# Kernel optimization log

Hardware: AMD Instinct MI355X
Metric: run time of the kernel (lower is better)

Reference implementation:

```python
import jax, jax.numpy as jnp
import numpy as np

N = 100000      # num nodes
E = 1600000     # num edges
DIN, DH, DOUT = 128, 64, 32
BN_EPS = 1e-5


def setup_inputs() -> dict:
    key = jax.random.key(0)
    ks = jax.random.split(key, 6)

    def xavier(k, fi, fo):
        lim = np.sqrt(6.0 / (fi + fo)).astype(np.float32)
        return jax.random.uniform(k, (fi, fo), jnp.float32, -lim, lim)

    return {
        "x": jax.random.normal(ks[0], (N, DIN), jnp.float32),
        "edge_index": jax.random.randint(ks[1], (2, E), 0, N, dtype=jnp.int32),
        "W1": xavier(ks[2], DIN, DH),
        "b1": jnp.zeros((DH,), jnp.float32),
        "gamma1": jnp.ones((DH,), jnp.float32),
        "beta1": jnp.zeros((DH,), jnp.float32),
        "W2": xavier(ks[3], DH, DOUT),
        "b2": jnp.zeros((DOUT,), jnp.float32),
    }


def _gcn_norm(edge_index, n, dtype):
    # add self-loops, then symmetric normalization deg^-1/2[src] * deg^-1/2[dst]
    loop = jnp.arange(n, dtype=edge_index.dtype)
    src = jnp.concatenate([edge_index[0], loop])
    dst = jnp.concatenate([edge_index[1], loop])
    deg = jax.ops.segment_sum(jnp.ones_like(dst, dtype=dtype), dst, num_segments=n)
    dis = 1.0 / jnp.sqrt(deg)  # deg >= 1 due to self-loops
    norm = dis[src] * dis[dst]
    return src, dst, norm


def _gcn_layer(h, W, b, src, dst, norm, n):
    h = h @ W
    msg = h[src] * norm[:, None]                       # [E+N, d] gather
    out = jax.ops.segment_sum(msg, dst, num_segments=n)  # scatter-add
    return out + b


def reference(x, edge_index, W1, b1, gamma1, beta1, W2, b2):
    src, dst, norm = _gcn_norm(edge_index, N, x.dtype)
    # layer 1: GCNConv -> BatchNorm (batch stats) -> ReLU (dropout = eval/identity)
    h = _gcn_layer(x, W1, b1, src, dst, norm, N)
    mean = h.mean(axis=0)
    var = h.var(axis=0)
    h = (h - mean) / jnp.sqrt(var + BN_EPS) * gamma1 + beta1
    h = jax.nn.relu(h)
    # layer 2: GCNConv -> node embeddings [N, DOUT]
    out = _gcn_layer(h, W2, b2, src, dst, norm, N)
    return out
```

## Files before the change

kernel.cpp:

```cpp
#include <hip/hip_runtime.h>

#define DIN 128
#define DH 64
#define DOUT 32
#define BN_EPS 1e-5f

#define BK 128
#define BKSH 7
#define NBK_MAX 784
#define G 256
#define CAP 2560
#define CCAP 3584

typedef __attribute__((ext_vector_type(8))) short short8;
typedef __attribute__((ext_vector_type(4))) float floatx4;

__device__ __forceinline__ unsigned short f2bf(float f) {
    union { float f; unsigned u; } v; v.f = f;
    unsigned r = (v.u + 0x7FFFu + ((v.u >> 16) & 1u)) >> 16;
    return (unsigned short)r;
}
__device__ __forceinline__ float bf2f(unsigned short h) {
    union { unsigned u; float f; } v; v.u = ((unsigned)h) << 16;
    return v.f;
}
__device__ __forceinline__ float lo_f(unsigned u) {
    union { unsigned u; float f; } v; v.u = u << 16;
    return v.f;
}
__device__ __forceinline__ float hi_f(unsigned u) {
    union { unsigned u; float f; } v; v.u = u & 0xFFFF0000u;
    return v.f;
}
__device__ __forceinline__ unsigned pack2bf(float lo, float hi) {
    return (unsigned)f2bf(lo) | ((unsigned)f2bf(hi) << 16);
}


__global__ __launch_bounds__(512) void hist_k(const int* __restrict__ dst, int* __restrict__ hist_g,
                                              int E, int nbk, int chunk) {
    __shared__ int hist[NBK_MAX];
    int g = blockIdx.x, tid = threadIdx.x;
    for (int b = tid; b < nbk; b += 512) hist[b] = 0;
    __syncthreads();
    int i0 = g * chunk, iend = min(i0 + chunk, E);
    for (int i = i0 + tid; i < iend; i += 512)
        atomicAdd(&hist[dst[i] >> BKSH], 1);
    __syncthreads();
    for (int b = tid; b < nbk; b += 512)
        hist_g[(size_t)g * nbk + b] = hist[b];
}


__global__ __launch_bounds__(256) void scan_k(const int* __restrict__ hist_g, int* __restrict__ rowoff,
                                              int* __restrict__ tot, int nbk) {
    __shared__ int seg[16][17];
    int tid = threadIdx.x;
    int gl = tid >> 4, bl = tid & 15;
    int b = blockIdx.x * 16 + bl;
    bool bok = b < nbk;
    int vals[16];
    int psum = 0;
    #pragma unroll
    for (int j = 0; j < 16; j++) {
        int g = gl * 16 + j;
        int v = bok ? hist_g[(size_t)g * nbk + b] : 0;
        vals[j] = v; psum += v;
    }
    seg[gl][bl] = psum;
    __syncthreads();
    #pragma unroll
    for (int off = 1; off < 16; off <<= 1) {
        int t = (gl >= off) ? seg[gl - off][bl] : 0;
        __syncthreads();
        seg[gl][bl] += t;
        __syncthreads();
    }
    int run = seg[gl][bl] - psum;
    if (gl == 15 && bok) tot[b] = seg[15][bl];
    #pragma unroll
    for (int j = 0; j < 16; j++) {
        int g = gl * 16 + j;
        if (bok) rowoff[(size_t)g * nbk + b] = run;
        run += vals[j];
    }
}


__global__ __launch_bounds__(512) void scatter_k(const int* __restrict__ src, const int* __restrict__ dst,
                                                 const int* __restrict__ rowoff,
                                                 unsigned* __restrict__ recs, int E, int nbk, int chunk) {
    __shared__ int cur[NBK_MAX];
    int g = blockIdx.x, tid = threadIdx.x;
    for (int b = tid; b < nbk; b += 512)
        cur[b] = b * CAP + rowoff[(size_t)g * nbk + b];
    __syncthreads();
    int i0 = g * chunk, iend = min(i0 + chunk, E);
    for (int i = i0 + tid; i < iend; i += 512) {
        int s = src[i], d = dst[i];
        int b = d >> BKSH;
        int slot = atomicAdd(&cur[b], 1);
        if (slot < (b + 1) * CAP)
            recs[slot] = ((unsigned)s << BKSH) | (unsigned)(d & (BK - 1));
    }
}


__global__ __launch_bounds__(512) void csr_k(const unsigned* __restrict__ recs, const int* __restrict__ tot,
                                             float* __restrict__ dis, int2* __restrict__ rpde,
                                             int* __restrict__ col, int n) {
    __shared__ int deg8[8][BK];
    __shared__ int wb[8][BK];
    __shared__ int deg[BK], sc[BK], bas[BK];
    int b = blockIdx.x, tid = threadIdx.x;
    int w = tid >> 6, lane = tid & 63;
    for (int i = tid; i < 8 * BK; i += 512) ((int*)deg8)[i] = 0;
    __syncthreads();
    int lo = b * CAP;
    int clo = b * CCAP;
    int ne = min(tot[b], CAP);
    int hi = lo + ne;
    for (int e = lo + w * 64 + lane; e < hi; e += 512)
        atomicAdd(&deg8[w][recs[e] & (BK - 1)], 1);
    __syncthreads();
    if (tid < BK) {
        int run = 0;
        #pragma unroll
        for (int ww = 0; ww < 8; ww++) { wb[ww][tid] = run; run += deg8[ww][tid]; }
        deg[tid] = run;
        sc[tid] = (run + 7) & ~7;
    }
    __syncthreads();
    for (int off = 1; off < BK; off <<= 1) {
        int t = (tid < BK && tid >= off) ? sc[tid - off] : 0;
        __syncthreads();
        if (tid < BK) sc[tid] += t;
        __syncthreads();
    }
    if (tid < BK) {
        int d = deg[tid];
        int pdeg = (d + 7) & ~7;
        int base = sc[tid] - pdeg;
        bas[tid] = base;
        int g = b * BK + tid;
        if (g < n) {
            dis[g] = rsqrtf((float)(d + 1));
            rpde[g] = make_int2(clo + base, d);
        }
        for (int j = d; j < pdeg; j++)
            col[clo + base + j] = n;
    }
    __syncthreads();
    for (int i = tid; i < 8 * BK; i += 512)
        ((int*)wb)[i] += bas[i & (BK - 1)];
    __syncthreads();
    for (int e = lo + w * 64 + lane; e < hi; e += 512) {
        unsigned r = recs[e];
        int dl = r & (BK - 1);
        int k = atomicAdd(&wb[w][dl], 1);
        col[clo + k] = (int)(r >> BKSH);
    }
}


__global__ __launch_bounds__(256) void gemm1_k(const float* __restrict__ x,
                                               const float* __restrict__ W1,
                                               const float* __restrict__ dis,
                                               unsigned short* __restrict__ h1s, int n, int np1) {
    __shared__ unsigned short xb[64][136];
    __shared__ unsigned short wt[64][136];
    int tid = threadIdx.x;
    int r0b = blockIdx.x * 64;

    for (int c = tid; c < 2048; c += 256) {
        int k = c >> 4, n4 = (c & 15) * 4;
        float4 v = ((const float4*)W1)[c];
        wt[n4 + 0][k] = f2bf(v.x);
        wt[n4 + 1][k] = f2bf(v.y);
        wt[n4 + 2][k] = f2bf(v.z);
        wt[n4 + 3][k] = f2bf(v.w);
    }
    for (int c = tid; c < 2048; c += 256) {
        int r = c >> 5, k4 = (c & 31) * 4;
        int gr = r0b + r;
        float4 v = make_float4(0.f, 0.f, 0.f, 0.f);
        if (gr < n) v = ((const float4*)x)[(gr << 5) + (k4 >> 2)];
        ushort4 o;
        o.x = f2bf(v.x); o.y = f2bf(v.y); o.z = f2bf(v.z); o.w = f2bf(v.w);
        *(ushort4*)&xb[r][k4] = o;
    }
    __syncthreads();

    int w = tid >> 6, lane = tid & 63;
    int rr = lane & 15, q = lane >> 4;
    floatx4 acc0 = {0.f, 0.f, 0.f, 0.f}, acc1 = acc0, acc2 = acc0, acc3 = acc0;
    #pragma unroll
    for (int kt = 0; kt < 4; kt++) {
        int k0 = kt * 32 + q * 8;
        short8 a  = *(const short8*)&xb[w * 16 + rr][k0];
        short8 b0 = *(const short8*)&wt[rr][k0];
        short8 b1 = *(const short8*)&wt[16 + rr][k0];
        short8 b2 = *(const short8*)&wt[32 + rr][k0];
        short8 b3 = *(const short8*)&wt[48 + rr][k0];
        acc0 = __builtin_amdgcn_mfma_f32_16x16x32_bf16(a, b0, acc0, 0, 0, 0);
        acc1 = __builtin_amdgcn_mfma_f32_16x16x32_bf16(a, b1, acc1, 0, 0, 0);
        acc2 = __builtin_amdgcn_mfma_f32_16x16x32_bf16(a, b2, acc2, 0, 0, 0);
        acc3 = __builtin_amdgcn_mfma_f32_16x16x32_bf16(a, b3, acc3, 0, 0, 0);
    }
    #pragma unroll
    for (int t = 0; t < 4; t++) {
        int gr = r0b + w * 16 + q * 4 + t;
        if (gr < n) {
            float dd = dis[gr];
            h1s[(size_t)0 * np1 * 16 + gr * 16 + rr] = f2bf(acc0[t] * dd);
            h1s[(size_t)1 * np1 * 16 + gr * 16 + rr] = f2bf(acc1[t] * dd);
            h1s[(size_t)2 * np1 * 16 + gr * 16 + rr] = f2bf(acc2[t] * dd);
            h1s[(size_t)3 * np1 * 16 + gr * 16 + rr] = f2bf(acc3[t] * dd);
        } else if (gr == n) {
            h1s[(size_t)0 * np1 * 16 + gr * 16 + rr] = 0;
            h1s[(size_t)1 * np1 * 16 + gr * 16 + rr] = 0;
            h1s[(size_t)2 * np1 * 16 + gr * 16 + rr] = 0;
            h1s[(size_t)3 * np1 * 16 + gr * 16 + rr] = 0;
        }
    }
}


__global__ __launch_bounds__(256) void agg1_k(const unsigned* __restrict__ h1p,
                                              const int2* __restrict__ rpde,
                                              const int* __restrict__ col,
                                              unsigned* __restrict__ outp, int n, int np1, int nh) {
    int b = blockIdx.x;
    int slot = b & 7;
    int q = slot >> 1, hn = slot & 1;
    int wv = threadIdx.x >> 6;
    int lane = threadIdx.x & 63;
    int half = lane >> 5, hl = lane & 31;
    int f = hl & 3, eslot = hl >> 2;
    int node = hn * nh + (b >> 3) * 8 + wv * 2 + half;
    if (node >= n) return;

    int2 rd = rpde[node];
    int e = rd.x, dg = rd.y;
    int pm = ((dg + 7) & ~7) - 1;

    const uint2* qt = (const uint2*)h1p + (size_t)q * np1 * 4;

    int i0 = eslot, i1 = 8 + eslot, i2 = 16 + eslot, i3 = 24 + eslot;
    int s0 = col[e + min(i0, pm)];
    int s1 = col[e + min(i1, pm)];
    int s2 = col[e + min(i2, pm)];
    int s3 = col[e + min(i3, pm)];
    s0 = (i0 <= pm) ? s0 : n;
    s1 = (i1 <= pm) ? s1 : n;
    s2 = (i2 <= pm) ? s2 : n;
    s3 = (i3 <= pm) ? s3 : n;
    uint2 u0 = qt[s0 * 4 + f];
    uint2 u1 = qt[s1 * 4 + f];
    uint2 u2 = qt[s2 * 4 + f];
    uint2 u3 = qt[s3 * 4 + f];
    uint2 us = qt[node * 4 + f];
    __builtin_amdgcn_sched_barrier(0);

    float xl = (lo_f(u0.x) + lo_f(u1.x)) + (lo_f(u2.x) + lo_f(u3.x));
    float xh = (hi_f(u0.x) + hi_f(u1.x)) + (hi_f(u2.x) + hi_f(u3.x));
    float yl = (lo_f(u0.y) + lo_f(u1.y)) + (lo_f(u2.y) + lo_f(u3.y));
    float yh = (hi_f(u0.y) + hi_f(u1.y)) + (hi_f(u2.y) + hi_f(u3.y));

    if (pm >= 32) {
        for (int bb = 32; bb <= pm; bb += 8) {
            int s = col[e + bb + eslot];
            uint2 u = qt[s * 4 + f];
            xl += lo_f(u.x); xh += hi_f(u.x);
            yl += lo_f(u.y); yh += hi_f(u.y);
        }
    }

    xl += __shfl_xor(xl, 4, 64); xl += __shfl_xor(xl, 8, 64); xl += __shfl_xor(xl, 16, 64);
    xh += __shfl_xor(xh, 4, 64); xh += __shfl_xor(xh, 8, 64); xh += __shfl_xor(xh, 16, 64);
    yl += __shfl_xor(yl, 4, 64); yl += __shfl_xor(yl, 8, 64); yl += __shfl_xor(yl, 16, 64);
    yh += __shfl_xor(yh, 4, 64); yh += __shfl_xor(yh, 8, 64); yh += __shfl_xor(yh, 16, 64);

    if (eslot == 0) {
        float dn = rsqrtf((float)(dg + 1));
        uint2 o;
        o.x = pack2bf((xl + lo_f(us.x)) * dn, (xh + hi_f(us.x)) * dn);
        o.y = pack2bf((yl + lo_f(us.y)) * dn, (yh + hi_f(us.y)) * dn);
        ((uint2*)outp)[((size_t)q * n + node) * 4 + f] = o;
    }
}


__global__ __launch_bounds__(256) void bnstats_k(const unsigned short* __restrict__ agg1b,
                                                 float* __restrict__ stats, int n) {
    int fidx = threadIdx.x & 63, g = threadIdx.x >> 6;
    int qq = fidx >> 4, fi = fidx & 15;
    const unsigned short* base = agg1b + (size_t)qq * n * 16 + fi;
    float sum = 0.f, sq = 0.f;
    for (int r = blockIdx.x * 4 + g; r < n; r += gridDim.x * 4) {
        float v = bf2f(base[(size_t)r * 16]);
        sum += v; sq += v * v;
    }
    __shared__ float s1[4][64], s2[4][64];
    s1[g][fidx] = sum; s2[g][fidx] = sq;
    __syncthreads();
    if (g == 0) {
        sum = s1[0][fidx] + s1[1][fidx] + s1[2][fidx] + s1[3][fidx];
        sq  = s2[0][fidx] + s2[1][fidx] + s2[2][fidx] + s2[3][fidx];
        atomicAdd(&stats[fidx], sum);
        atomicAdd(&stats[64 + fidx], sq);
    }
}


__global__ __launch_bounds__(256) void gemm2_k(const unsigned short* __restrict__ agg1b,
                                               const float* __restrict__ W2,
                                               const float* __restrict__ stats,
                                               const float* __restrict__ gamma, const float* __restrict__ beta,
                                               const float* __restrict__ dis,
                                               unsigned short* __restrict__ h2s, float invn, int n, int np1) {
    __shared__ unsigned short ab[64][72];
    __shared__ unsigned short wt[32][72];
    __shared__ float s_s[64], s_t[64];
    int tid = threadIdx.x;
    int r0b = blockIdx.x * 64;
    if (tid < 64) {
        float mean = stats[tid] * invn;
        float var = stats[64 + tid] * invn - mean * mean;
        float s = gamma[tid] * rsqrtf(var + BN_EPS);
        s_s[tid] = s;
        s_t[tid] = beta[tid] - mean * s;
    }
    for (int c = tid; c < 512; c += 256) {
        int k = c >> 3, n4 = (c & 7) * 4;
        float4 v = ((const float4*)W2)[c];
        wt[n4 + 0][k] = f2bf(v.x);
        wt[n4 + 1][k] = f2bf(v.y);
        wt[n4 + 2][k] = f2bf(v.z);
        wt[n4 + 3][k] = f2bf(v.w);
    }
    __syncthreads();
    for (int c = tid; c < 512; c += 256) {
        int r = c >> 3, k0 = (c & 7) * 8;
        int gr = r0b + r;
        unsigned short tmp[8];
        if (gr < n) {
            const unsigned short* ap = &agg1b[(size_t)(k0 >> 4) * n * 16 + gr * 16 + (k0 & 8)];
            #pragma unroll
            for (int j = 0; j < 8; j++)
                tmp[j] = f2bf(fmaxf(bf2f(ap[j]) * s_s[k0 + j] + s_t[k0 + j], 0.f));
        } else {
            #pragma unroll
            for (int j = 0; j < 8; j++) tmp[j] = 0;
        }
        *(short8*)&ab[r][k0] = *(short8*)tmp;
    }
    __syncthreads();

    int w = tid >> 6, lane = tid & 63;
    int rr = lane & 15, q = lane >> 4;
    floatx4 acc0 = {0.f, 0.f, 0.f, 0.f}, acc1 = acc0;
    #pragma unroll
    for (int kt = 0; kt < 2; kt++) {
        int k0 = kt * 32 + q * 8;
        short8 a  = *(const short8*)&ab[w * 16 + rr][k0];
        short8 b0 = *(const short8*)&wt[rr][k0];
        short8 b1 = *(const short8*)&wt[16 + rr][k0];
        acc0 = __builtin_amdgcn_mfma_f32_16x16x32_bf16(a, b0, acc0, 0, 0, 0);
        acc1 = __builtin_amdgcn_mfma_f32_16x16x32_bf16(a, b1, acc1, 0, 0, 0);
    }
    #pragma unroll
    for (int t = 0; t < 4; t++) {
        int gr = r0b + w * 16 + q * 4 + t;
        if (gr < n) {
            float dd = dis[gr];
            h2s[(size_t)0 * np1 * 16 + gr * 16 + rr] = f2bf(acc0[t] * dd);
            h2s[(size_t)1 * np1 * 16 + gr * 16 + rr] = f2bf(acc1[t] * dd);
        } else if (gr == n) {
            h2s[(size_t)0 * np1 * 16 + gr * 16 + rr] = 0;
            h2s[(size_t)1 * np1 * 16 + gr * 16 + rr] = 0;
        }
    }
}


__global__ __launch_bounds__(256) void agg2_k(const unsigned* __restrict__ h2p,
                                              const int2* __restrict__ rpde,
                                              const int* __restrict__ col, const float* __restrict__ b2,
                                              float* __restrict__ out, int n, int np1, int nq) {
    int b = blockIdx.x;
    int slot = b & 7;
    int h = slot >> 2, qn = slot & 3;
    int wv = threadIdx.x >> 6;
    int lane = threadIdx.x & 63;
    int half = lane >> 5, hl = lane & 31;
    int f = hl & 3, eslot = hl >> 2;
    int node = qn * nq + (b >> 3) * 8 + wv * 2 + half;
    if (node >= n) return;

    int2 rd = rpde[node];
    int e = rd.x, dg = rd.y;
    int pm = ((dg + 7) & ~7) - 1;

    const uint2* ht = (const uint2*)h2p + (size_t)h * np1 * 4;

    int i0 = eslot, i1 = 8 + eslot, i2 = 16 + eslot, i3 = 24 + eslot;
    int s0 = col[e + min(i0, pm)];
    int s1 = col[e + min(i1, pm)];
    int s2 = col[e + min(i2, pm)];
    int s3 = col[e + min(i3, pm)];
    s0 = (i0 <= pm) ? s0 : n;
    s1 = (i1 <= pm) ? s1 : n;
    s2 = (i2 <= pm) ? s2 : n;
    s3 = (i3 <= pm) ? s3 : n;
    uint2 u0 = ht[s0 * 4 + f];
    uint2 u1 = ht[s1 * 4 + f];
    uint2 u2 = ht[s2 * 4 + f];
    uint2 u3 = ht[s3 * 4 + f];
    uint2 us = ht[node * 4 + f];
    __builtin_amdgcn_sched_barrier(0);

    float xl = (lo_f(u0.x) + lo_f(u1.x)) + (lo_f(u2.x) + lo_f(u3.x));
    float xh = (hi_f(u0.x) + hi_f(u1.x)) + (hi_f(u2.x) + hi_f(u3.x));
    float yl = (lo_f(u0.y) + lo_f(u1.y)) + (lo_f(u2.y) + lo_f(u3.y));
    float yh = (hi_f(u0.y) + hi_f(u1.y)) + (hi_f(u2.y) + hi_f(u3.y));

    if (pm >= 32) {
        for (int bb = 32; bb <= pm; bb += 8) {
            int s = col[e + bb + eslot];
            uint2 u = ht[s * 4 + f];
            xl += lo_f(u.x); xh += hi_f(u.x);
            yl += lo_f(u.y); yh += hi_f(u.y);
        }
    }

    xl += __shfl_xor(xl, 4, 64); xl += __shfl_xor(xl, 8, 64); xl += __shfl_xor(xl, 16, 64);
    xh += __shfl_xor(xh, 4, 64); xh += __shfl_xor(xh, 8, 64); xh += __shfl_xor(xh, 16, 64);
    yl += __shfl_xor(yl, 4, 64); yl += __shfl_xor(yl, 8, 64); yl += __shfl_xor(yl, 16, 64);
    yh += __shfl_xor(yh, 4, 64); yh += __shfl_xor(yh, 8, 64); yh += __shfl_xor(yh, 16, 64);

    if (eslot == 0) {
        float dn = rsqrtf((float)(dg + 1));
        float4 bb4 = ((const float4*)b2)[h * 4 + f];
        float4 o;
        o.x = (xl + lo_f(us.x)) * dn + bb4.x;
        o.y = (xh + hi_f(us.x)) * dn + bb4.y;
        o.z = (yl + lo_f(us.y)) * dn + bb4.z;
        o.w = (yh + hi_f(us.y)) * dn + bb4.w;
        ((float4*)out)[(size_t)node * 8 + h * 4 + f] = o;
    }
}


extern "C" void kernel_launch(void* const* d_in, const int* in_sizes, int n_in,
                              void* d_out, int out_size, void* d_ws, size_t ws_size,
                              hipStream_t stream) {
    const float* x      = (const float*)d_in[0];
    const int*   ei     = (const int*)d_in[1];
    const float* W1     = (const float*)d_in[2];
    const float* gamma1 = (const float*)d_in[4];
    const float* beta1  = (const float*)d_in[5];
    const float* W2     = (const float*)d_in[6];
    const float* b2     = (const float*)d_in[7];
    float* out = (float*)d_out;

    int N = in_sizes[0] / DIN;
    int E = in_sizes[1] / 2;
    const int* src = ei;
    const int* dst = ei + E;
    int nbk = (N + BK - 1) >> BKSH;
    int chunk = (E + G - 1) / G;
    int np1 = N + 1;

    size_t off = 0;
    auto alloc = [&](size_t elems) -> void* {
        void* p = (char*)d_ws + off * 4;
        off += (elems + 127) & ~size_t(127);
        return p;
    };
    int*            hist_g = (int*)alloc((size_t)G * NBK_MAX);
    int*            rowoff = (int*)alloc((size_t)G * NBK_MAX);
    int*            tot    = (int*)alloc(NBK_MAX);
    unsigned*       recs   = (unsigned*)alloc((size_t)NBK_MAX * CAP);
    int*            col    = (int*)alloc((size_t)NBK_MAX * CCAP);
    float*          dis    = (float*)alloc(N);
    int2*           rpde   = (int2*)alloc((size_t)N * 2);
    float*          stats  = (float*)alloc(128);
    unsigned short* h1s    = (unsigned short*)alloc((size_t)np1 * DH / 2);
    unsigned short* agg1b  = (unsigned short*)alloc((size_t)N * DH / 2);
    unsigned short* h2s    = h1s;

    hipMemsetAsync(stats, 0, 128 * sizeof(float), stream);

    hist_k<<<G, 512, 0, stream>>>(dst, hist_g, E, nbk, chunk);
    scan_k<<<(nbk + 15) / 16, 256, 0, stream>>>(hist_g, rowoff, tot, nbk);
    scatter_k<<<G, 512, 0, stream>>>(src, dst, rowoff, recs, E, nbk, chunk);
    csr_k<<<nbk, 512, 0, stream>>>(recs, tot, dis, rpde, col, N);

    gemm1_k<<<(N + 63) / 64, 256, 0, stream>>>(x, W1, dis, h1s, N, np1);

    int nh = (N + 1) / 2;
    int agg1_blocks = 8 * ((nh + 7) / 8);
    agg1_k<<<agg1_blocks, 256, 0, stream>>>((const unsigned*)h1s, rpde, col, (unsigned*)agg1b,
                                            N, np1, nh);

    bnstats_k<<<400, 256, 0, stream>>>(agg1b, stats, N);

    gemm2_k<<<(N + 63) / 64, 256, 0, stream>>>(agg1b, W2, stats, gamma1, beta1, dis, h2s,
                                               1.0f / (float)N, N, np1);

    int nqn = (N + 3) / 4;
    int agg2_blocks = 8 * ((nqn + 7) / 8);
    agg2_k<<<agg2_blocks, 256, 0, stream>>>((const unsigned*)h2s, rpde, col, b2, out,
                                            N, np1, nqn);
}
```

Baseline: 288.7 us.

## Assign one node per 4-lane group in aggregation kernels, dropping cross-lane reductions

The aggregation kernels now map 16 nodes per wavefront, with 4 lanes per node each owning a feature chunk. Each lane walks all of its node's edges serially in unrolled groups of 8, up to the wave-wide maximum degree, so the shuffle reductions go away. CSR padding becomes (d+8)&~7 so every row has at least one pad entry, which lets overrun indices clamp onto it. This trades intra-node edge parallelism for more nodes per wave and fewer reductions, but a single high-degree node now stalls its whole wave (degree divergence), and per-lane load latency chains get longer.

Measured after the change: 271.6 us. 5.9% less time.

```diff
diff --git a/kernel.cpp b/kernel.cpp
--- a/kernel.cpp
+++ b/kernel.cpp
@@ -128,7 +128,7 @@
         #pragma unroll
         for (int ww = 0; ww < 8; ww++) { wb[ww][tid] = run; run += deg8[ww][tid]; }
         deg[tid] = run;
-        sc[tid] = (run + 7) & ~7;
+        sc[tid] = (run + 8) & ~7;
     }
     __syncthreads();
     for (int off = 1; off < BK; off <<= 1) {
@@ -139,7 +139,7 @@
     }
     if (tid < BK) {
         int d = deg[tid];
-        int pdeg = (d + 7) & ~7;
+        int pdeg = (d + 8) & ~7;
         int base = sc[tid] - pdeg;
         bas[tid] = base;
         int g = b * BK + tid;
@@ -235,57 +235,41 @@
     int q = slot >> 1, hn = slot & 1;
     int wv = threadIdx.x >> 6;
     int lane = threadIdx.x & 63;
-    int half = lane >> 5, hl = lane & 31;
-    int f = hl & 3, eslot = hl >> 2;
-    int node = hn * nh + (b >> 3) * 8 + wv * 2 + half;
-    if (node >= n) return;
-
-    int2 rd = rpde[node];
-    int e = rd.x, dg = rd.y;
-    int pm = ((dg + 7) & ~7) - 1;
+    int ns = lane >> 2, f = lane & 3;
+    int node = hn * nh + (b >> 3) * 64 + wv * 16 + ns;
+    bool ok = node < n;
+    int nd = ok ? node : n;
+
+    int2 rd = rpde[ok ? node : 0];
+    int e = rd.x;
+    int dg = ok ? rd.y : 0;
+    int pdg = (dg + 8) & ~7;
+    int pm = pdg - 1;
+
+    int itmax = pdg;
+    itmax = max(itmax, __shfl_xor(itmax, 4, 64));
+    itmax = max(itmax, __shfl_xor(itmax, 8, 64));
+    itmax = max(itmax, __shfl_xor(itmax, 16, 64));
+    itmax = max(itmax, __shfl_xor(itmax, 32, 64));
 
     const uint2* qt = (const uint2*)h1p + (size_t)q * np1 * 4;
-
-    int i0 = eslot, i1 = 8 + eslot, i2 = 16 + eslot, i3 = 24 + eslot;
-    int s0 = col[e + min(i0, pm)];
-    int s1 = col[e + min(i1, pm)];
-    int s2 = col[e + min(i2, pm)];
-    int s3 = col[e + min(i3, pm)];
-    s0 = (i0 <= pm) ? s0 : n;
-    s1 = (i1 <= pm) ? s1 : n;
-    s2 = (i2 <= pm) ? s2 : n;
-    s3 = (i3 <= pm) ? s3 : n;
-    uint2 u0 = qt[s0 * 4 + f];
-    uint2 u1 = qt[s1 * 4 + f];
-    uint2 u2 = qt[s2 * 4 + f];
-    uint2 u3 = qt[s3 * 4 + f];
-    uint2 us = qt[node * 4 + f];
-    __builtin_amdgcn_sched_barrier(0);
-
-    float xl = (lo_f(u0.x) + lo_f(u1.x)) + (lo_f(u2.x) + lo_f(u3.x));
-    float xh = (hi_f(u0.x) + hi_f(u1.x)) + (hi_f(u2.x) + hi_f(u3.x));
-    float yl = (lo_f(u0.y) + lo_f(u1.y)) + (lo_f(u2.y) + lo_f(u3.y));
-    float yh = (hi_f(u0.y) + hi_f(u1.y)) + (hi_f(u2.y) + hi_f(u3.y));
-
-    if (pm >= 32) {
-        for (int bb = 32; bb <= pm; bb += 8) {
-            int s = col[e + bb + eslot];
-            uint2 u = qt[s * 4 + f];
-            xl += lo_f(u.x); xh += hi_f(u.x);
-            yl += lo_f(u.y); yh += hi_f(u.y);
-        }
-    }
-
-    xl += __shfl_xor(xl, 4, 64); xl += __shfl_xor(xl, 8, 64); xl += __shfl_xor(xl, 16, 64);
-    xh += __shfl_xor(xh, 4, 64); xh += __shfl_xor(xh, 8, 64); xh += __shfl_xor(xh, 16, 64);
-    yl += __shfl_xor(yl, 4, 64); yl += __shfl_xor(yl, 8, 64); yl += __shfl_xor(yl, 16, 64);
-    yh += __shfl_xor(yh, 4, 64); yh += __shfl_xor(yh, 8, 64); yh += __shfl_xor(yh, 16, 64);
-
-    if (eslot == 0) {
+    float s0 = 0.f, s1 = 0.f, s2 = 0.f, s3 = 0.f;
+    for (int i = 0; i < itmax; i += 8) {
+        #pragma unroll
+        for (int j = 0; j < 8; j++) {
+            int c = col[e + min(i + j, pm)];
+            uint2 u = qt[c * 4 + f];
+            s0 += lo_f(u.x); s1 += hi_f(u.x);
+            s2 += lo_f(u.y); s3 += hi_f(u.y);
+        }
+    }
+
+    uint2 us = qt[nd * 4 + f];
+    if (ok) {
         float dn = rsqrtf((float)(dg + 1));
         uint2 o;
-        o.x = pack2bf((xl + lo_f(us.x)) * dn, (xh + hi_f(us.x)) * dn);
-        o.y = pack2bf((yl + lo_f(us.y)) * dn, (yh + hi_f(us.y)) * dn);
+        o.x = pack2bf((s0 + lo_f(us.x)) * dn, (s1 + hi_f(us.x)) * dn);
+        o.y = pack2bf((s2 + lo_f(us.y)) * dn, (s3 + hi_f(us.y)) * dn);
         ((uint2*)outp)[((size_t)q * n + node) * 4 + f] = o;
     }
 }
@@ -393,60 +377,44 @@
     int h = slot >> 2, qn = slot & 3;
     int wv = threadIdx.x >> 6;
     int lane = threadIdx.x & 63;
-    int half = lane >> 5, hl = lane & 31;
-    int f = hl & 3, eslot = hl >> 2;
-    int node = qn * nq + (b >> 3) * 8 + wv * 2 + half;
-    if (node >= n) return;
-
-    int2 rd = rpde[node];
-    int e = rd.x, dg = rd.y;
-    int pm = ((dg + 7) & ~7) - 1;
+    int ns = lane >> 2, f = lane & 3;
+    int node = qn * nq + (b >> 3) * 64 + wv * 16 + ns;
+    bool ok = node < n;
+    int nd = ok ? node : n;
+
+    int2 rd = rpde[ok ? node : 0];
+    int e = rd.x;
+    int dg = ok ? rd.y : 0;
+    int pdg = (dg + 8) & ~7;
+    int pm = pdg - 1;
+
+    int itmax = pdg;
+    itmax = max(itmax, __shfl_xor(itmax, 4, 64));
+    itmax = max(itmax, __shfl_xor(itmax, 8, 64));
+    itmax = max(itmax, __shfl_xor(itmax, 16, 64));
+    itmax = max(itmax, __shfl_xor(itmax, 32, 64));
 
     const uint2* ht = (const uint2*)h2p + (size_t)h * np1 * 4;
-
-    int i0 = eslot, i1 = 8 + eslot, i2 = 16 + eslot, i3 = 24 + eslot;
-    int s0 = col[e + min(i0, pm)];
-    int s1 = col[e + min(i1, pm)];
-    int s2 = col[e + min(i2, pm)];
-    int s3 = col[e + min(i3, pm)];
-    s0 = (i0 <= pm) ? s0 : n;
-    s1 = (i1 <= pm) ? s1 : n;
-    s2 = (i2 <= pm) ? s2 : n;
-    s3 = (i3 <= pm) ? s3 : n;
-    uint2 u0 = ht[s0 * 4 + f];
-    uint2 u1 = ht[s1 * 4 + f];
-    uint2 u2 = ht[s2 * 4 + f];
-    uint2 u3 = ht[s3 * 4 + f];
-    uint2 us = ht[node * 4 + f];
-    __builtin_amdgcn_sched_barrier(0);
-
-    float xl = (lo_f(u0.x) + lo_f(u1.x)) + (lo_f(u2.x) + lo_f(u3.x));
-    float xh = (hi_f(u0.x) + hi_f(u1.x)) + (hi_f(u2.x) + hi_f(u3.x));
-    float yl = (lo_f(u0.y) + lo_f(u1.y)) + (lo_f(u2.y) + lo_f(u3.y));
-    float yh = (hi_f(u0.y) + hi_f(u1.y)) + (hi_f(u2.y) + hi_f(u3.y));
-
-    if (pm >= 32) {
-        for (int bb = 32; bb <= pm; bb += 8) {
-            int s = col[e + bb + eslot];
-            uint2 u = ht[s * 4 + f];
-            xl += lo_f(u.x); xh += hi_f(u.x);
-            yl += lo_f(u.y); yh += hi_f(u.y);
-        }
-    }
-
-    xl += __shfl_xor(xl, 4, 64); xl += __shfl_xor(xl, 8, 64); xl += __shfl_xor(xl, 16, 64);
-    xh += __shfl_xor(xh, 4, 64); xh += __shfl_xor(xh, 8, 64); xh += __shfl_xor(xh, 16, 64);
-    yl += __shfl_xor(yl, 4, 64); yl += __shfl_xor(yl, 8, 64); yl += __shfl_xor(yl, 16, 64);
-    yh += __shfl_xor(yh, 4, 64); yh += __shfl_xor(yh, 8, 64); yh += __shfl_xor(yh, 16, 64);
-
-    if (eslot == 0) {
+    float s0 = 0.f, s1 = 0.f, s2 = 0.f, s3 = 0.f;
+    for (int i = 0; i < itmax; i += 8) {
+        #pragma unroll
+        for (int j = 0; j < 8; j++) {
+            int c = col[e + min(i + j, pm)];
+            uint2 u = ht[c * 4 + f];
+            s0 += lo_f(u.x); s1 += hi_f(u.x);
+            s2 += lo_f(u.y); s3 += hi_f(u.y);
+        }
+    }
+
+    uint2 us = ht[nd * 4 + f];
+    if (ok) {
         float dn = rsqrtf((float)(dg + 1));
-        float4 bb4 = ((const float4*)b2)[h * 4 + f];
+        float4 bb = ((const float4*)b2)[h * 4 + f];
         float4 o;
-        o.x = (xl + lo_f(us.x)) * dn + bb4.x;
-        o.y = (xh + hi_f(us.x)) * dn + bb4.y;
-        o.z = (yl + lo_f(us.y)) * dn + bb4.z;
-        o.w = (yh + hi_f(us.y)) * dn + bb4.w;
+        o.x = (s0 + lo_f(us.x)) * dn + bb.x;
+        o.y = (s1 + hi_f(us.x)) * dn + bb.y;
+        o.z = (s2 + lo_f(us.y)) * dn + bb.z;
+        o.w = (s3 + hi_f(us.y)) * dn + bb.w;
         ((float4*)out)[(size_t)node * 8 + h * 4 + f] = o;
     }
 }
@@ -500,7 +468,7 @@
     gemm1_k<<<(N + 63) / 64, 256, 0, stream>>>(x, W1, dis, h1s, N, np1);
 
     int nh = (N + 1) / 2;
-    int agg1_blocks = 8 * ((nh + 7) / 8);
+    int agg1_blocks = 8 * ((nh + 63) / 64);
     agg1_k<<<agg1_blocks, 256, 0, stream>>>((const unsigned*)h1s, rpde, col, (unsigned*)agg1b,
                                             N, np1, nh);
 
@@ -510,7 +478,7 @@
                                                1.0f / (float)N, N, np1);
 
     int nqn = (N + 3) / 4;
-    int agg2_blocks = 8 * ((nqn + 7) / 8);
+    int agg2_blocks = 8 * ((nqn + 63) / 64);
     agg2_k<<<agg2_blocks, 256, 0, stream>>>((const unsigned*)h2s, rpde, col, b2, out,
                                             N, np1, nqn);
 }
```
